# Performance work log

Hardware: AMD Instinct MI355X
Metric: run time of the kernel (lower is better)

Reference implementation:

```python
import jax, jax.numpy as jnp
from jax import lax
import numpy as np

K = 3
PAD = (K - 1) // 2
EPS = 1e-5


def setup_inputs() -> dict:
    key = jax.random.key(0)
    k0, k1, k2, k3 = jax.random.split(key, 4)
    B, C, O, H, W = 8, 128, 128, 64, 64
    x = jax.random.normal(k0, (B, C, H, W), jnp.float32)
    bn_gamma = jnp.ones((C,), jnp.float32)
    bn_beta = jnp.zeros((C,), jnp.float32)
    bn_mean = jnp.zeros((C,), jnp.float32)
    bn_var = jnp.ones((C,), jnp.float32)
    # small offset-conv weights -> realistic sub-pixel offsets
    w_off = jax.random.normal(k1, (2 * K * K, C, K, K), jnp.float32) * 0.01
    b_off = jnp.zeros((2 * K * K,), jnp.float32)
    w_dconv = jax.random.normal(k2, (O, C, K, K), jnp.float32) * (1.0 / np.sqrt(C * K * K))
    b_dconv = jax.random.normal(k3, (O,), jnp.float32) * 0.01
    return dict(x=x, bn_gamma=bn_gamma, bn_beta=bn_beta, bn_mean=bn_mean,
                bn_var=bn_var, w_off=w_off, b_off=b_off,
                w_dconv=w_dconv, b_dconv=b_dconv)


def _conv2d(x, w, b):
    y = lax.conv_general_dilated(
        x, w, window_strides=(1, 1), padding=[(PAD, PAD), (PAD, PAD)],
        dimension_numbers=('NCHW', 'OIHW', 'NCHW'))
    return y + b[None, :, None, None]


def _deform_conv2d(x, offsets, w, b):
    # torchvision DeformConv2d semantics (deform_groups=1, groups=1, stride=1)
    B, C, H, W = x.shape
    KK = K * K
    off = offsets.reshape(B, KK, 2, H, W)  # (dy, dx) per kernel tap
    dy, dx = off[:, :, 0], off[:, :, 1]    # [B,KK,H,W]
    kh = (jnp.arange(KK) // K).astype(x.dtype)
    kw = (jnp.arange(KK) % K).astype(x.dtype)
    # sampling positions: p0 + pk - pad + offset
    py = dy + jnp.arange(H, dtype=x.dtype)[None, None, :, None] + (kh - PAD)[None, :, None, None]
    px = dx + jnp.arange(W, dtype=x.dtype)[None, None, None, :] + (kw - PAD)[None, :, None, None]
    y0 = jnp.floor(py)
    x0 = jnp.floor(px)
    wy = py - y0
    wx = px - x0
    y0i = y0.astype(jnp.int32)
    x0i = x0.astype(jnp.int32)
    xflat = x.reshape(B, C, H * W)

    def gather(yi, xi):
        valid = (yi >= 0) & (yi < H) & (xi >= 0) & (xi < W)
        idx = jnp.clip(yi, 0, H - 1) * W + jnp.clip(xi, 0, W - 1)  # [B,KK,H,W]
        vals = jax.vmap(lambda xf, ii: xf[:, ii])(xflat, idx)      # [B,C,KK,H,W]
        return vals * valid[:, None].astype(x.dtype)

    # bilinear sample with implicit zero padding outside the image
    v = (((1 - wy) * (1 - wx))[:, None] * gather(y0i, x0i)
         + ((1 - wy) * wx)[:, None] * gather(y0i, x0i + 1)
         + (wy * (1 - wx))[:, None] * gather(y0i + 1, x0i)
         + (wy * wx)[:, None] * gather(y0i + 1, x0i + 1))  # [B,C,KK,H,W]
    out = jnp.einsum('bckhw,ock->bohw', v, w.reshape(w.shape[0], C, KK))
    return out + b[None, :, None, None]


def reference(x, bn_gamma, bn_beta, bn_mean, bn_var, w_off, b_off, w_dconv, b_dconv):
    # BN (inference form) + ReLU
    inv = bn_gamma * lax.rsqrt(bn_var + EPS)
    h = jnp.maximum((x - bn_mean[None, :, None, None]) * inv[None, :, None, None]
                    + bn_beta[None, :, None, None], 0.0)
    offsets = _conv2d(h, w_off, b_off)          # [B, 2*K*K, H, W]
    return _deform_conv2d(h, offsets, w_dconv, b_dconv)
```

## Files before the change

### kernel.cpp

```cpp
#include <hip/hip_runtime.h>

#define CC 128
#define OO 128
#define HH 64
#define WW 64
#define HW (HH*WW)

typedef __attribute__((ext_vector_type(8))) __bf16 bf16x8;
typedef __attribute__((ext_vector_type(4))) __bf16 bf16x4;
typedef __attribute__((ext_vector_type(4))) float  f32x4;

__global__ __launch_bounds__(256) void prep(
    const float* __restrict__ x,
    const float* __restrict__ gamma, const float* __restrict__ beta,
    const float* __restrict__ mean,  const float* __restrict__ var,
    const float* __restrict__ w_dconv, const float* __restrict__ w_off,
    __bf16* __restrict__ h,
    __bf16* __restrict__ wt_swz,
    __bf16* __restrict__ woff_swz)
{
    __shared__ float inv_s[128], bb_s[128];
    __shared__ __bf16 tile[64 * 130];
    int blk = blockIdx.x;
    int tid = threadIdx.x;

    if (blk >= 512) {
        int idx = (blk - 512) * 256 + tid;
        if (idx < 147456) {
            int j    = idx & 7;
            int lane = (idx >> 3) & 63;
            int og   = (idx >> 9) & 7;
            int ks   = (idx >> 12) & 3;
            int kk   = idx >> 14;
            int o = og * 16 + (lane & 15);
            int c = ks * 32 + (lane >> 4) * 8 + j;
            wt_swz[idx] = (__bf16)w_dconv[(o * 128 + c) * 9 + kk];
        }
        if (idx < 36864) {
            int j    = idx & 7;
            int lane = (idx >> 3) & 63;
            int og   = (idx >> 9) & 1;
            int ks   = (idx >> 10) & 3;
            int kk   = idx >> 12;
            int o = og * 16 + (lane & 15);
            int c = ks * 32 + (lane >> 4) * 8 + j;
            float v = (o < 18) ? w_off[o * 1152 + c * 9 + kk] : 0.f;
            woff_swz[idx] = (__bf16)v;
        }
        return;
    }

    int b = blk & 7, y = blk >> 3;
    if (tid < 128) {
        float iv = gamma[tid] * rsqrtf(var[tid] + 1e-5f);
        inv_s[tid] = iv;
        bb_s[tid]  = beta[tid] - mean[tid] * iv;
    }
    __syncthreads();

    const float* xb = x + (size_t)b * CC * HW + (size_t)y * WW;
    #pragma unroll
    for (int i = 0; i < 8; ++i) {
        int idx = i * 256 + tid;
        int c = idx >> 4, x4 = idx & 15;
        float4 v = *(const float4*)(xb + (size_t)c * HW + x4 * 4);
        float iv = inv_s[c], bb = bb_s[c];
        tile[(x4 * 4 + 0) * 130 + c] = (__bf16)fmaxf(v.x * iv + bb, 0.f);
        tile[(x4 * 4 + 1) * 130 + c] = (__bf16)fmaxf(v.y * iv + bb, 0.f);
        tile[(x4 * 4 + 2) * 130 + c] = (__bf16)fmaxf(v.z * iv + bb, 0.f);
        tile[(x4 * 4 + 3) * 130 + c] = (__bf16)fmaxf(v.w * iv + bb, 0.f);
    }
    __syncthreads();

    __bf16* hb = h + ((size_t)b * HW + (size_t)y * WW) * CC;
    #pragma unroll
    for (int i = 0; i < 2; ++i) {
        int idx = i * 256 + tid;
        int xx = idx >> 3, c16 = idx & 7;
        const uint* src = (const uint*)&tile[xx * 130 + c16 * 16];
        uint r0 = src[0], r1 = src[1], r2 = src[2], r3 = src[3];
        uint r4 = src[4], r5 = src[5], r6 = src[6], r7 = src[7];
        uint* dst = (uint*)(hb + (size_t)xx * CC + c16 * 16);
        *(uint4*)dst       = (uint4){r0, r1, r2, r3};
        *(uint4*)(dst + 4) = (uint4){r4, r5, r6, r7};
    }
}

__global__ __launch_bounds__(256, 3) void fused_mfma(
    const __bf16* __restrict__ h,
    const __bf16* __restrict__ woff_swz,
    const float* __restrict__ b_off,
    const __bf16* __restrict__ wt_swz,
    const float* __restrict__ b_dconv,
    float* __restrict__ out)
{
    __shared__ float pw[576 * 4];
    __shared__ ushort pidx[576 * 4];
    __shared__ __align__(16) __bf16 vt[2][64 * 136];
    __shared__ float offs_lds[18 * 64];

    int blk = blockIdx.x;
    int b = blk & 7, y = blk >> 3;
    int tid = threadIdx.x;
    int lane = tid & 63;
    int wv  = __builtin_amdgcn_readfirstlane(tid >> 6);
    int l15 = lane & 15, quad = lane >> 4;

    const __bf16* hb = h + (size_t)b * HW * CC;

    {
        const bf16x8* w8 = (const bf16x8*)woff_swz;

        f32x4 acc[2];
        acc[0] = (f32x4){0.f, 0.f, 0.f, 0.f};
        acc[1] = (f32x4){0.f, 0.f, 0.f, 0.f};

        uint4 pa[4];
        {
            int yy = y - 1;
            bool yok = (yy >= 0);
            #pragma unroll
            for (int i = 0; i < 4; ++i) {
                int idx = i * 256 + tid;
                int xx = idx >> 4, c8 = idx & 15;
                int xs = xx - 1;
                pa[i] = (uint4){0u, 0u, 0u, 0u};
                if (yok && xs >= 0)
                    pa[i] = *(const uint4*)(hb + ((size_t)yy * WW + xs) * CC + c8 * 8);
            }
        }

        for (int kk = 0; kk < 9; ++kk) {
            int buf = kk & 1;
            #pragma unroll
            for (int i = 0; i < 4; ++i) {
                int idx = i * 256 + tid;
                int xx = idx >> 4, c8 = idx & 15;
                *(uint4*)&vt[buf][xx * 136 + c8 * 8] = pa[i];
            }
            if (kk < 8) {
                int k2 = kk + 1;
                int dy = k2 / 3 - 1, dx = k2 % 3 - 1;
                int yy = y + dy;
                bool yok = (yy >= 0) && (yy < HH);
                #pragma unroll
                for (int i = 0; i < 4; ++i) {
                    int idx = i * 256 + tid;
                    int xx = idx >> 4, c8 = idx & 15;
                    int xs = xx + dx;
                    pa[i] = (uint4){0u, 0u, 0u, 0u};
                    if (yok && xs >= 0 && xs < WW)
                        pa[i] = *(const uint4*)(hb + ((size_t)yy * WW + xs) * CC + c8 * 8);
                }
            }
            asm volatile("s_waitcnt lgkmcnt(0)" ::: "memory");
            __builtin_amdgcn_s_barrier();
            #pragma unroll
            for (int ks = 0; ks < 4; ++ks) {
                int kb = ks * 32 + quad * 8;
                bf16x8 a  = *(const bf16x8*)&vt[buf][(wv * 16 + l15) * 136 + kb];
                bf16x8 b0 = w8[((kk * 4 + ks) * 2 + 0) * 64 + lane];
                bf16x8 b1 = w8[((kk * 4 + ks) * 2 + 1) * 64 + lane];
                acc[0] = __builtin_amdgcn_mfma_f32_16x16x32_bf16(a, b0, acc[0], 0, 0, 0);
                acc[1] = __builtin_amdgcn_mfma_f32_16x16x32_bf16(a, b1, acc[1], 0, 0, 0);
            }
        }

        #pragma unroll
        for (int nt = 0; nt < 2; ++nt) {
            int oc = nt * 16 + l15;
            if (oc < 18) {
                float bias = b_off[oc];
                #pragma unroll
                for (int r = 0; r < 4; ++r) {
                    int xx = wv * 16 + quad * 4 + r;
                    offs_lds[oc * 64 + xx] = acc[nt][r] + bias;
                }
            }
        }
    }
    __syncthreads();

    for (int e = tid; e < 576; e += 256) {
        int kk = e >> 6, xx = e & 63;
        float dy = offs_lds[(2 * kk) * 64 + xx];
        float dx = offs_lds[(2 * kk + 1) * 64 + xx];
        float py = dy + (float)y + (float)(kk / 3 - 1);
        float px = dx + (float)xx + (float)(kk % 3 - 1);
        float fy = floorf(py), fx = floorf(px);
        int y0 = (int)fy, x0 = (int)fx;
        float wy = py - fy, wx = px - fx;
        int y1 = y0 + 1, x1 = x0 + 1;
        bool vy0 = (y0 >= 0) && (y0 < HH);
        bool vy1 = (y1 >= 0) && (y1 < HH);
        bool vx0 = (x0 >= 0) && (x0 < WW);
        bool vx1 = (x1 >= 0) && (x1 < WW);
        int yc0 = min(max(y0, 0), HH - 1), yc1 = min(max(y1, 0), HH - 1);
        int xc0 = min(max(x0, 0), WW - 1), xc1 = min(max(x1, 0), WW - 1);
        pw[e * 4 + 0] = (vy0 && vx0) ? (1.f - wy) * (1.f - wx) : 0.f;
        pw[e * 4 + 1] = (vy0 && vx1) ? (1.f - wy) * wx         : 0.f;
        pw[e * 4 + 2] = (vy1 && vx0) ? wy * (1.f - wx)         : 0.f;
        pw[e * 4 + 3] = (vy1 && vx1) ? wy * wx                 : 0.f;
        pidx[e * 4 + 0] = (ushort)(yc0 * WW + xc0);
        pidx[e * 4 + 1] = (ushort)(yc0 * WW + xc1);
        pidx[e * 4 + 2] = (ushort)(yc1 * WW + xc0);
        pidx[e * 4 + 3] = (ushort)(yc1 * WW + xc1);
    }
    __syncthreads();

    const bf16x8* w8 = (const bf16x8*)wt_swz;

    f32x4 acc[4][2];
    #pragma unroll
    for (int mt = 0; mt < 4; ++mt)
        #pragma unroll
        for (int nt = 0; nt < 2; ++nt)
            acc[mt][nt] = (f32x4){0.f, 0.f, 0.f, 0.f};

    bf16x8 pt0[4], pt1[4], pt2[4], pt3[4];
    #pragma unroll
    for (int i = 0; i < 4; ++i) {
        int idx = i * 256 + tid;
        int xx = idx >> 4, c8 = idx & 15;
        int e = xx;
        pt0[i] = *(const bf16x8*)(hb + ((int)pidx[e * 4 + 0] << 7) + c8 * 8);
        pt1[i] = *(const bf16x8*)(hb + ((int)pidx[e * 4 + 1] << 7) + c8 * 8);
        pt2[i] = *(const bf16x8*)(hb + ((int)pidx[e * 4 + 2] << 7) + c8 * 8);
        pt3[i] = *(const bf16x8*)(hb + ((int)pidx[e * 4 + 3] << 7) + c8 * 8);
    }

    for (int kk = 0; kk < 9; ++kk) {
        int buf = kk & 1;
        #pragma unroll
        for (int i = 0; i < 4; ++i) {
            int idx = i * 256 + tid;
            int xx = idx >> 4, c8 = idx & 15;
            int e = (kk << 6) + xx;
            float w0 = pw[e * 4 + 0], w1 = pw[e * 4 + 1];
            float w2 = pw[e * 4 + 2], w3 = pw[e * 4 + 3];
            bf16x8 pk;
            #pragma unroll
            for (int q = 0; q < 8; ++q) {
                float v = w0 * (float)pt0[i][q] + w1 * (float)pt1[i][q]
                        + w2 * (float)pt2[i][q] + w3 * (float)pt3[i][q];
                pk[q] = (__bf16)v;
            }
            *(bf16x8*)&vt[buf][xx * 136 + c8 * 8] = pk;
        }
        if (kk < 8) {
            #pragma unroll
            for (int i = 0; i < 4; ++i) {
                int idx = i * 256 + tid;
                int xx = idx >> 4, c8 = idx & 15;
                int e2 = ((kk + 1) << 6) + xx;
                pt0[i] = *(const bf16x8*)(hb + ((int)pidx[e2 * 4 + 0] << 7) + c8 * 8);
                pt1[i] = *(const bf16x8*)(hb + ((int)pidx[e2 * 4 + 1] << 7) + c8 * 8);
                pt2[i] = *(const bf16x8*)(hb + ((int)pidx[e2 * 4 + 2] << 7) + c8 * 8);
                pt3[i] = *(const bf16x8*)(hb + ((int)pidx[e2 * 4 + 3] << 7) + c8 * 8);
            }
        }
        asm volatile("s_waitcnt lgkmcnt(0)" ::: "memory");
        __builtin_amdgcn_s_barrier();
        #pragma unroll
        for (int ks = 0; ks < 4; ++ks) {
            int kb = ks * 32 + quad * 8;
            bf16x8 b0 = w8[((kk * 4 + ks) * 8 + 2 * wv + 0) * 64 + lane];
            bf16x8 b1 = w8[((kk * 4 + ks) * 8 + 2 * wv + 1) * 64 + lane];
            bf16x8 a0 = *(const bf16x8*)&vt[buf][(0 * 16 + l15) * 136 + kb];
            bf16x8 a1 = *(const bf16x8*)&vt[buf][(1 * 16 + l15) * 136 + kb];
            bf16x8 a2 = *(const bf16x8*)&vt[buf][(2 * 16 + l15) * 136 + kb];
            bf16x8 a3 = *(const bf16x8*)&vt[buf][(3 * 16 + l15) * 136 + kb];
            acc[0][0] = __builtin_amdgcn_mfma_f32_16x16x32_bf16(a0, b0, acc[0][0], 0, 0, 0);
            acc[1][0] = __builtin_amdgcn_mfma_f32_16x16x32_bf16(a1, b0, acc[1][0], 0, 0, 0);
            acc[2][0] = __builtin_amdgcn_mfma_f32_16x16x32_bf16(a2, b0, acc[2][0], 0, 0, 0);
            acc[3][0] = __builtin_amdgcn_mfma_f32_16x16x32_bf16(a3, b0, acc[3][0], 0, 0, 0);
            acc[0][1] = __builtin_amdgcn_mfma_f32_16x16x32_bf16(a0, b1, acc[0][1], 0, 0, 0);
            acc[1][1] = __builtin_amdgcn_mfma_f32_16x16x32_bf16(a1, b1, acc[1][1], 0, 0, 0);
            acc[2][1] = __builtin_amdgcn_mfma_f32_16x16x32_bf16(a2, b1, acc[2][1], 0, 0, 0);
            acc[3][1] = __builtin_amdgcn_mfma_f32_16x16x32_bf16(a3, b1, acc[3][1], 0, 0, 0);
        }
    }

    size_t ob = (size_t)b * OO * HW + (size_t)y * WW;
    #pragma unroll
    for (int nt = 0; nt < 2; ++nt) {
        int o = wv * 32 + nt * 16 + l15;
        float bias = b_dconv[o];
        #pragma unroll
        for (int mt = 0; mt < 4; ++mt) {
            int xb = mt * 16 + quad * 4;
            float4 r;
            r.x = acc[mt][nt][0] + bias;
            r.y = acc[mt][nt][1] + bias;
            r.z = acc[mt][nt][2] + bias;
            r.w = acc[mt][nt][3] + bias;
            *(float4*)&out[ob + (size_t)o * HW + xb] = r;
        }
    }
}

extern "C" void kernel_launch(void* const* d_in, const int* in_sizes, int n_in,
                              void* d_out, int out_size, void* d_ws, size_t ws_size,
                              hipStream_t stream)
{
    const float* x       = (const float*)d_in[0];
    const float* gamma   = (const float*)d_in[1];
    const float* beta    = (const float*)d_in[2];
    const float* mean    = (const float*)d_in[3];
    const float* var     = (const float*)d_in[4];
    const float* w_off   = (const float*)d_in[5];
    const float* b_off   = (const float*)d_in[6];
    const float* w_dconv = (const float*)d_in[7];
    const float* b_dconv = (const float*)d_in[8];
    float* out = (float*)d_out;

    char* ws = (char*)d_ws;
    __bf16* h_bf     = (__bf16*)ws;
    __bf16* wt_swz   = (__bf16*)(ws + 8388608);
    __bf16* woff_swz = (__bf16*)(ws + 8683520);

    prep<<<1232, 256, 0, stream>>>(x, gamma, beta, mean, var,
                                   w_dconv, w_off, h_bf, wt_swz, woff_swz);
    fused_mfma<<<512, 256, 0, stream>>>(h_bf, woff_swz, b_off,
                                        wt_swz, b_dconv, out);
}
```

Measured before the change: 121.6 us.

## Double fused kernel block to 512 threads, splitting output channels across eight waves

The fused deformable-conv kernel now runs 8 waves per block instead of 4. In the offset conv, each wave computes one 16x16 tile (4 pixel tiles by 2 channel groups). In the main GEMM, each wave owns 16 output channels instead of 32. Gather loads and LDS staging are split over twice as many threads, which halves per-thread registers and is meant to raise occupancy and hide gather latency. The cost is larger blocks and more barrier participants, while LDS per block stays the same.

```diff
diff --git a/kernel.cpp b/kernel.cpp
--- a/kernel.cpp
+++ b/kernel.cpp
@@ -86,7 +86,7 @@
     }
 }
 
-__global__ __launch_bounds__(256, 3) void fused_mfma(
+__global__ __launch_bounds__(512, 4) void fused_mfma(
     const __bf16* __restrict__ h,
     const __bf16* __restrict__ woff_swz,
     const float* __restrict__ b_off,
@@ -110,18 +110,18 @@
 
     {
         const bf16x8* w8 = (const bf16x8*)woff_swz;
-
-        f32x4 acc[2];
-        acc[0] = (f32x4){0.f, 0.f, 0.f, 0.f};
-        acc[1] = (f32x4){0.f, 0.f, 0.f, 0.f};
-
-        uint4 pa[4];
+        int ma = wv & 3;
+        int oga = wv >> 2;
+
+        f32x4 acc = (f32x4){0.f, 0.f, 0.f, 0.f};
+
+        uint4 pa[2];
         {
             int yy = y - 1;
             bool yok = (yy >= 0);
             #pragma unroll
-            for (int i = 0; i < 4; ++i) {
-                int idx = i * 256 + tid;
+            for (int i = 0; i < 2; ++i) {
+                int idx = i * 512 + tid;
                 int xx = idx >> 4, c8 = idx & 15;
                 int xs = xx - 1;
                 pa[i] = (uint4){0u, 0u, 0u, 0u};
@@ -133,8 +133,8 @@
         for (int kk = 0; kk < 9; ++kk) {
             int buf = kk & 1;
             #pragma unroll
-            for (int i = 0; i < 4; ++i) {
-                int idx = i * 256 + tid;
+            for (int i = 0; i < 2; ++i) {
+                int idx = i * 512 + tid;
                 int xx = idx >> 4, c8 = idx & 15;
                 *(uint4*)&vt[buf][xx * 136 + c8 * 8] = pa[i];
             }
@@ -144,8 +144,8 @@
                 int yy = y + dy;
                 bool yok = (yy >= 0) && (yy < HH);
                 #pragma unroll
-                for (int i = 0; i < 4; ++i) {
-                    int idx = i * 256 + tid;
+                for (int i = 0; i < 2; ++i) {
+                    int idx = i * 512 + tid;
                     int xx = idx >> 4, c8 = idx & 15;
                     int xs = xx + dx;
                     pa[i] = (uint4){0u, 0u, 0u, 0u};
@@ -158,30 +158,27 @@
             #pragma unroll
             for (int ks = 0; ks < 4; ++ks) {
                 int kb = ks * 32 + quad * 8;
-                bf16x8 a  = *(const bf16x8*)&vt[buf][(wv * 16 + l15) * 136 + kb];
-                bf16x8 b0 = w8[((kk * 4 + ks) * 2 + 0) * 64 + lane];
-                bf16x8 b1 = w8[((kk * 4 + ks) * 2 + 1) * 64 + lane];
-                acc[0] = __builtin_amdgcn_mfma_f32_16x16x32_bf16(a, b0, acc[0], 0, 0, 0);
-                acc[1] = __builtin_amdgcn_mfma_f32_16x16x32_bf16(a, b1, acc[1], 0, 0, 0);
-            }
-        }
-
-        #pragma unroll
-        for (int nt = 0; nt < 2; ++nt) {
-            int oc = nt * 16 + l15;
+                bf16x8 a  = *(const bf16x8*)&vt[buf][(ma * 16 + l15) * 136 + kb];
+                bf16x8 b0 = w8[((kk * 4 + ks) * 2 + oga) * 64 + lane];
+                acc = __builtin_amdgcn_mfma_f32_16x16x32_bf16(a, b0, acc, 0, 0, 0);
+            }
+        }
+
+        {
+            int oc = oga * 16 + l15;
             if (oc < 18) {
                 float bias = b_off[oc];
                 #pragma unroll
                 for (int r = 0; r < 4; ++r) {
-                    int xx = wv * 16 + quad * 4 + r;
-                    offs_lds[oc * 64 + xx] = acc[nt][r] + bias;
+                    int xx = ma * 16 + quad * 4 + r;
+                    offs_lds[oc * 64 + xx] = acc[r] + bias;
                 }
             }
         }
     }
     __syncthreads();
 
-    for (int e = tid; e < 576; e += 256) {
+    for (int e = tid; e < 576; e += 512) {
         int kk = e >> 6, xx = e & 63;
         float dy = offs_lds[(2 * kk) * 64 + xx];
         float dx = offs_lds[(2 * kk + 1) * 64 + xx];
@@ -210,17 +207,15 @@
 
     const bf16x8* w8 = (const bf16x8*)wt_swz;
 
-    f32x4 acc[4][2];
+    f32x4 acc[4];
     #pragma unroll
     for (int mt = 0; mt < 4; ++mt)
-        #pragma unroll
-        for (int nt = 0; nt < 2; ++nt)
-            acc[mt][nt] = (f32x4){0.f, 0.f, 0.f, 0.f};
-
-    bf16x8 pt0[4], pt1[4], pt2[4], pt3[4];
+        acc[mt] = (f32x4){0.f, 0.f, 0.f, 0.f};
+
+    bf16x8 pt0[2], pt1[2], pt2[2], pt3[2];
     #pragma unroll
-    for (int i = 0; i < 4; ++i) {
-        int idx = i * 256 + tid;
+    for (int i = 0; i < 2; ++i) {
+        int idx = i * 512 + tid;
         int xx = idx >> 4, c8 = idx & 15;
         int e = xx;
         pt0[i] = *(const bf16x8*)(hb + ((int)pidx[e * 4 + 0] << 7) + c8 * 8);
@@ -232,8 +227,8 @@
     for (int kk = 0; kk < 9; ++kk) {
         int buf = kk & 1;
         #pragma unroll
-        for (int i = 0; i < 4; ++i) {
-            int idx = i * 256 + tid;
+        for (int i = 0; i < 2; ++i) {
+            int idx = i * 512 + tid;
             int xx = idx >> 4, c8 = idx & 15;
             int e = (kk << 6) + xx;
             float w0 = pw[e * 4 + 0], w1 = pw[e * 4 + 1];
@@ -249,8 +244,8 @@
         }
         if (kk < 8) {
             #pragma unroll
-            for (int i = 0; i < 4; ++i) {
-                int idx = i * 256 + tid;
+            for (int i = 0; i < 2; ++i) {
+                int idx = i * 512 + tid;
                 int xx = idx >> 4, c8 = idx & 15;
                 int e2 = ((kk + 1) << 6) + xx;
                 pt0[i] = *(const bf16x8*)(hb + ((int)pidx[e2 * 4 + 0] << 7) + c8 * 8);
@@ -264,36 +259,30 @@
         #pragma unroll
         for (int ks = 0; ks < 4; ++ks) {
             int kb = ks * 32 + quad * 8;
-            bf16x8 b0 = w8[((kk * 4 + ks) * 8 + 2 * wv + 0) * 64 + lane];
-            bf16x8 b1 = w8[((kk * 4 + ks) * 8 + 2 * wv + 1) * 64 + lane];
+            bf16x8 b0 = w8[((kk * 4 + ks) * 8 + wv) * 64 + lane];
             bf16x8 a0 = *(const bf16x8*)&vt[buf][(0 * 16 + l15) * 136 + kb];
             bf16x8 a1 = *(const bf16x8*)&vt[buf][(1 * 16 + l15) * 136 + kb];
             bf16x8 a2 = *(const bf16x8*)&vt[buf][(2 * 16 + l15) * 136 + kb];
             bf16x8 a3 = *(const bf16x8*)&vt[buf][(3 * 16 + l15) * 136 + kb];
-            acc[0][0] = __builtin_amdgcn_mfma_f32_16x16x32_bf16(a0, b0, acc[0][0], 0, 0, 0);
-            acc[1][0] = __builtin_amdgcn_mfma_f32_16x16x32_bf16(a1, b0, acc[1][0], 0, 0, 0);
-            acc[2][0] = __builtin_amdgcn_mfma_f32_16x16x32_bf16(a2, b0, acc[2][0], 0, 0, 0);
-            acc[3][0] = __builtin_amdgcn_mfma_f32_16x16x32_bf16(a3, b0, acc[3][0], 0, 0, 0);
-            acc[0][1] = __builtin_amdgcn_mfma_f32_16x16x32_bf16(a0, b1, acc[0][1], 0, 0, 0);
-            acc[1][1] = __builtin_amdgcn_mfma_f32_16x16x32_bf16(a1, b1, acc[1][1], 0, 0, 0);
-            acc[2][1] = __builtin_amdgcn_mfma_f32_16x16x32_bf16(a2, b1, acc[2][1], 0, 0, 0);
-            acc[3][1] = __builtin_amdgcn_mfma_f32_16x16x32_bf16(a3, b1, acc[3][1], 0, 0, 0);
+            acc[0] = __builtin_amdgcn_mfma_f32_16x16x32_bf16(a0, b0, acc[0], 0, 0, 0);
+            acc[1] = __builtin_amdgcn_mfma_f32_16x16x32_bf16(a1, b0, acc[1], 0, 0, 0);
+            acc[2] = __builtin_amdgcn_mfma_f32_16x16x32_bf16(a2, b0, acc[2], 0, 0, 0);
+            acc[3] = __builtin_amdgcn_mfma_f32_16x16x32_bf16(a3, b0, acc[3], 0, 0, 0);
         }
     }
 
     size_t ob = (size_t)b * OO * HW + (size_t)y * WW;
-    #pragma unroll
-    for (int nt = 0; nt < 2; ++nt) {
-        int o = wv * 32 + nt * 16 + l15;
+    {
+        int o = wv * 16 + l15;
         float bias = b_dconv[o];
         #pragma unroll
         for (int mt = 0; mt < 4; ++mt) {
             int xb = mt * 16 + quad * 4;
             float4 r;
-            r.x = acc[mt][nt][0] + bias;
-            r.y = acc[mt][nt][1] + bias;
-            r.z = acc[mt][nt][2] + bias;
-            r.w = acc[mt][nt][3] + bias;
+            r.x = acc[mt][0] + bias;
+            r.y = acc[mt][1] + bias;
+            r.z = acc[mt][2] + bias;
+            r.w = acc[mt][3] + bias;
             *(float4*)&out[ob + (size_t)o * HW + xb] = r;
         }
     }
@@ -321,6 +310,6 @@
 
     prep<<<1232, 256, 0, stream>>>(x, gamma, beta, mean, var,
                                    w_dconv, w_off, h_bf, wt_swz, woff_swz);
-    fused_mfma<<<512, 256, 0, stream>>>(h_bf, woff_swz, b_off,
+    fused_mfma<<<512, 512, 0, stream>>>(h_bf, woff_swz, b_off,
                                         wt_swz, b_dconv, out);
 }
```

After: 117.7 us. 1.03x faster.
